# Performance work log

Hardware: AMD Instinct MI355X
Metric: run time of the kernel (lower is better)

## Reference

```python
import jax, jax.numpy as jnp
import numpy as np

N_HEAD = 32
N_KV_HEAD = 8
HEAD_DIM = 64
ROPE_THETA = 10000.0


def apply_rope(x):
    # x: [B, H, T, D], interleaved-pair RoPE (rotary_embedding_torch style)
    B, H, T, D = x.shape
    inv_freq = 1.0 / (ROPE_THETA ** (jnp.arange(0, D, 2, dtype=jnp.float32) / D))  # [D/2]
    ang = jnp.arange(T, dtype=jnp.float32)[:, None] * inv_freq[None, :]  # [T, D/2]
    cos = jnp.cos(ang)[None, None].astype(x.dtype)  # [1,1,T,D/2]
    sin = jnp.sin(ang)[None, None].astype(x.dtype)
    xe = x[..., 0::2]
    xo = x[..., 1::2]
    re = xe * cos - xo * sin
    ro = xo * cos + xe * sin
    return jnp.stack([re, ro], axis=-1).reshape(B, H, T, D)


def setup_inputs() -> dict:
    key = jax.random.key(0)
    ks = jax.random.split(key, 5)
    B, T, C = 2, 2048, 2048
    kv_dim = N_KV_HEAD * HEAD_DIM
    s = 0.02
    return {
        "x": jax.random.normal(ks[0], (B, T, C), jnp.float32),
        "wq": jax.random.normal(ks[1], (C, C), jnp.float32) * s,
        "wk": jax.random.normal(ks[2], (C, kv_dim), jnp.float32) * s,
        "wv": jax.random.normal(ks[3], (C, kv_dim), jnp.float32) * s,
        "wo": jax.random.normal(ks[4], (C, C), jnp.float32) * s,
    }


def reference(x, wq, wk, wv, wo):
    B, T, C = x.shape
    hd = HEAD_DIM
    q = (x @ wq).reshape(B, T, N_HEAD, hd).transpose(0, 2, 1, 3)      # [B,H,T,d]
    k = (x @ wk).reshape(B, T, N_KV_HEAD, hd).transpose(0, 2, 1, 3)   # [B,Hkv,T,d]
    v = (x @ wv).reshape(B, T, N_KV_HEAD, hd).transpose(0, 2, 1, 3)
    q = apply_rope(q)
    k = apply_rope(k)
    rep = N_HEAD // N_KV_HEAD
    k = jnp.repeat(k, rep, axis=1)  # repeat_interleave over head dim
    v = jnp.repeat(v, rep, axis=1)
    att = jnp.einsum('bhqd,bhkd->bhqk', q, k) * (1.0 / np.sqrt(hd))
    causal = jnp.tril(jnp.ones((T, T), dtype=bool))
    att = jnp.where(causal[None, None], att, jnp.finfo(att.dtype).min)
    att = jax.nn.softmax(att, axis=-1)
    y = jnp.einsum('bhqk,bhkd->bhqd', att, v)
    y = y.transpose(0, 2, 1, 3).reshape(B, T, C)
    return y @ wo
```

## Files before the change

kernel.cpp:

```cpp
#include <hip/hip_runtime.h>
#include <hip/hip_bf16.h>
#include <cstdint>
#include <cstddef>


using bf16 = __hip_bfloat16;
using f32x4  = __attribute__((ext_vector_type(4))) float;
using f32x16 = __attribute__((ext_vector_type(16))) float;
using short8 = __attribute__((ext_vector_type(8))) short;
using u32x4  = __attribute__((ext_vector_type(4))) unsigned int;

typedef __attribute__((address_space(1))) const void* gp1_t;
typedef __attribute__((address_space(3))) void*       lp3_t;

#define GLOAD_LDS16(g, l)                                                     \
  __builtin_amdgcn_global_load_lds((gp1_t)(const void*)(g), (lp3_t)(void*)(l), 16, 0, 0)

#define MFMA32(a, b, c) __builtin_amdgcn_mfma_f32_32x32x16_bf16(a, b, c, 0, 0, 0)

static constexpr int Bd  = 2;
static constexpr int Td  = 2048;
static constexpr int Cd  = 2048;
static constexpr int NH  = 32;
static constexpr int NKV = 8;
static constexpr int HD  = 64;
static constexpr int Md  = Bd * Td;

__device__ inline float bf2f(unsigned short u) {
  union { unsigned int i; float f; } v; v.i = ((unsigned int)u) << 16; return v.f;
}
__device__ inline unsigned short f2bfbits(float f) {
  union { float f; unsigned int u; } v; v.f = f;
  unsigned int r = v.u + 0x7fffu + ((v.u >> 16) & 1u);
  return (unsigned short)(r >> 16);
}
__device__ inline unsigned int pkbf(float a, float b) {
  unsigned int r;
  asm("v_cvt_pk_bf16_f32 %0, %1, %2" : "=v"(r) : "v"(a), "v"(b));
  return r;
}
__device__ inline void plswapf(float& a, float& b) {
  asm("v_permlane32_swap_b32 %0, %1" : "+v"(a), "+v"(b));
}
__device__ inline void plswapu(unsigned int& a, unsigned int& b) {
  asm("v_permlane32_swap_b32 %0, %1" : "+v"(a), "+v"(b));
}
__device__ inline float hmax16(const f32x16& v) {
  float a0 = fmaxf(v[0], v[1]),   a1 = fmaxf(v[2], v[3]);
  float a2 = fmaxf(v[4], v[5]),   a3 = fmaxf(v[6], v[7]);
  float a4 = fmaxf(v[8], v[9]),   a5 = fmaxf(v[10], v[11]);
  float a6 = fmaxf(v[12], v[13]), a7 = fmaxf(v[14], v[15]);
  float b0 = fmaxf(a0, a1), b1 = fmaxf(a2, a3);
  float b2 = fmaxf(a4, a5), b3 = fmaxf(a6, a7);
  return fmaxf(fmaxf(b0, b1), fmaxf(b2, b3));
}
__device__ inline float hsum16(const f32x16& v) {
  float a0 = v[0]+v[1],   a1 = v[2]+v[3],   a2 = v[4]+v[5],   a3 = v[6]+v[7];
  float a4 = v[8]+v[9],   a5 = v[10]+v[11], a6 = v[12]+v[13], a7 = v[14]+v[15];
  float b0 = a0+a1, b1 = a2+a3, b2 = a4+a5, b3 = a6+a7;
  return (b0+b1)+(b2+b3);
}

__global__ __launch_bounds__(256) void prep1_kernel(const float* __restrict__ x,
                                                    const float* __restrict__ wq,
                                                    const float* __restrict__ wk,
                                                    const float* __restrict__ wv,
                                                    bf16* __restrict__ xb,
                                                    bf16* __restrict__ w1) {
  __shared__ float tile[32][33];
  int bid = blockIdx.x, tid = threadIdx.x;
  if (bid < 8192) {
    int i = bid * 256 + tid;
    float4 v = ((const float4*)x)[i];
    ushort4 o;
    o.x = f2bfbits(v.x); o.y = f2bfbits(v.y); o.z = f2bfbits(v.z); o.w = f2bfbits(v.w);
    ((ushort4*)xb)[i] = o;
    return;
  }
  const float* in; bf16* out; int Cc, bx, by;
  if (bid < 12288)      { int l = bid - 8192;  in = wq; out = w1;                        Cc = 2048; bx = l & 63; by = l >> 6; }
  else if (bid < 13312) { int l = bid - 12288; in = wk; out = w1 + (size_t)2048 * 2048;  Cc = 512;  bx = l & 15; by = l >> 4; }
  else                  { int l = bid - 13312; in = wv; out = w1 + (size_t)2560 * 2048;  Cc = 512;  bx = l & 15; by = l >> 4; }
  int tx = tid & 31, ty = tid >> 5;
  int col = bx * 32 + tx;
#pragma unroll
  for (int i = 0; i < 4; ++i) {
    int row = by * 32 + ty + i * 8;
    tile[ty + i * 8][tx] = in[(size_t)row * Cc + col];
  }
  __syncthreads();
#pragma unroll
  for (int i = 0; i < 4; ++i) {
    int orow = bx * 32 + ty + i * 8;
    int ocol = by * 32 + tx;
    out[(size_t)orow * 2048 + ocol] = __float2bfloat16(tile[tx][ty + i * 8]);
  }
}

__global__ __launch_bounds__(256) void transpose_f2b(const float* __restrict__ in,
                                                     bf16* __restrict__ out,
                                                     int R, int Cc) {
  __shared__ float tile[32][33];
  int tx = threadIdx.x & 31, ty = threadIdx.x >> 5;
  int bx = blockIdx.x, by = blockIdx.y;
  int col = bx * 32 + tx;
#pragma unroll
  for (int i = 0; i < 4; ++i) {
    int row = by * 32 + ty + i * 8;
    tile[ty + i * 8][tx] = in[(size_t)row * Cc + col];
  }
  __syncthreads();
#pragma unroll
  for (int i = 0; i < 4; ++i) {
    int orow = bx * 32 + ty + i * 8;
    int ocol = by * 32 + tx;
    out[(size_t)orow * R + ocol] = __float2bfloat16(tile[tx][ty + i * 8]);
  }
}

template <int MODE>
__global__ __launch_bounds__(256, 2) void gemm_bf16(const bf16* __restrict__ A,
                                                    const bf16* __restrict__ Bt,
                                                    void* __restrict__ Cp,
                                                    int M, int N, int K) {
  __shared__ __align__(16) bf16 Al[2][128 * 64];
  __shared__ __align__(16) bf16 Bl[2][128 * 64];
  int tid = threadIdx.x;
  int w = tid >> 6, lane = tid & 63;
  int lr = lane & 15, lg = lane >> 4;
  int m0 = blockIdx.x * 128, n0 = blockIdx.y * 128;
  int wr = w >> 1, wc = w & 1;
  f32x4 acc[4][4] = {};

  size_t Kb = (size_t)K * 2;
  int c8 = lane & 7, r8 = lane >> 3;
  const char* Asrc = (const char*)A + (size_t)(m0 + w * 8 + r8) * Kb + ((c8 ^ r8) << 4);
  const char* Bsrc = (const char*)Bt + (size_t)(n0 + w * 8 + r8) * Kb + ((c8 ^ r8) << 4);

#define GSTAGE(kt, bb) do {                                                   \
    char* ald = (char*)&Al[bb][0] + w * 1024;                                 \
    char* bld = (char*)&Bl[bb][0] + w * 1024;                                 \
    _Pragma("unroll")                                                         \
    for (int j = 0; j < 4; ++j) {                                             \
      GLOAD_LDS16(Asrc + (size_t)j * 32 * Kb + (size_t)(kt) * 2, ald + j * 4096); \
      GLOAD_LDS16(Bsrc + (size_t)j * 32 * Kb + (size_t)(kt) * 2, bld + j * 4096); \
    }                                                                         \
  } while (0)

  int nkt = K >> 6;
  GSTAGE(0, 0);
  asm volatile("s_waitcnt vmcnt(0)" ::: "memory");
  __builtin_amdgcn_s_barrier();
  __builtin_amdgcn_sched_barrier(0);

  for (int t = 0; t < nkt; ++t) {
    int cur = t & 1;
    if (t + 1 < nkt) {
      GSTAGE((t + 1) << 6, cur ^ 1);
      asm volatile("s_waitcnt vmcnt(8)" ::: "memory");
    } else {
      asm volatile("s_waitcnt vmcnt(0)" ::: "memory");
    }
    __builtin_amdgcn_s_barrier();
    __builtin_amdgcn_sched_barrier(0);
    const char* Ab = (const char*)&Al[cur][0];
    const char* Bb = (const char*)&Bl[cur][0];
    __builtin_amdgcn_s_setprio(1);
#pragma unroll
    for (int kk = 0; kk < 2; ++kk) {
      short8 af[4], bfr[4];
#pragma unroll
      for (int f = 0; f < 4; ++f) {
        int ra = wr * 64 + f * 16 + lr;
        int rb = wc * 64 + f * 16 + lr;
        int cb = (((kk << 2) | lg) ^ (lr & 7)) << 4;
        af[f]  = *(const short8*)(Ab + (size_t)ra * 128 + cb);
        bfr[f] = *(const short8*)(Bb + (size_t)rb * 128 + cb);
      }
#pragma unroll
      for (int i = 0; i < 4; ++i)
#pragma unroll
        for (int j = 0; j < 4; ++j)
          acc[i][j] = __builtin_amdgcn_mfma_f32_16x16x32_bf16(af[i], bfr[j], acc[i][j], 0, 0, 0);
    }
    __builtin_amdgcn_s_setprio(0);
    asm volatile("s_waitcnt lgkmcnt(0)" ::: "memory");
    __builtin_amdgcn_sched_barrier(0);
    __builtin_amdgcn_s_barrier();
  }
#undef GSTAGE

  bf16* Qb  = (bf16*)Cp;
  bf16* Kb2 = Qb + (size_t)Bd * NH * Td * HD;
  bf16* Vtb = Kb2 + (size_t)Bd * NKV * Td * HD;

  if (MODE == 3 && n0 >= 2560) {
    int h  = (n0 - 2560 + wc * 64) >> 6;
    int b  = m0 >> 11;
    int tg = (m0 & 2047) + wr * 64;
    char* tb = (w < 2 ? (char*)&Al[0][0] : (char*)&Bl[0][0]) + (w & 1) * 8192;
#pragma unroll
    for (int i = 0; i < 4; ++i)
#pragma unroll
      for (int j = 0; j < 4; ++j)
#pragma unroll
        for (int r = 0; r < 4; r += 2) {
          int d  = j * 16 + lr;
          int tt = i * 16 + lg * 4 + r;
          unsigned int pk = pkbf(acc[i][j][r], acc[i][j][r + 1]);
          *(unsigned int*)(tb + (((size_t)d * 128 + tt * 2) ^ ((d & 7) << 4))) = pk;
        }
    asm volatile("s_waitcnt lgkmcnt(0)" ::: "memory");
    __builtin_amdgcn_sched_barrier(0);
    char* Vdst = (char*)Vtb + ((((size_t)b * NKV + h) * 64) * Td + tg) * 2;
#pragma unroll
    for (int p = 0; p < 8; ++p) {
      int d  = p * 8 + (lane >> 3);
      int tc = lane & 7;
      u32x4 v = *(const u32x4*)(tb + (((size_t)d * 128 + tc * 16) ^ ((d & 7) << 4)));
      *(u32x4*)(Vdst + (size_t)d * Td * 2 + tc * 16) = v;
    }
    return;
  }

  if (MODE == 3) {
    const float RC = -0.41524101186092029f;
    float sc = (n0 < 2048) ? 0.18033688011112042f : 1.0f;
    int odd = lane & 1;
#pragma unroll
    for (int j = 0; j < 4; ++j) {
      int ncol = n0 + wc * 64 + j * 16 + lr;
      int d  = ncol & 63;
      float inv = __builtin_amdgcn_exp2f((float)(d >> 1) * RC);
#pragma unroll
      for (int i = 0; i < 4; ++i) {
#pragma unroll
        for (int r = 0; r < 4; ++r) {
          int mrow = m0 + wr * 64 + i * 16 + lg * 4 + r;
          int t = mrow & 2047;
          float v = acc[i][j][r];
          float p = __shfl_xor(v, 1);
          float rev = (float)t * inv * 0.15915494309189535f;
          rev = rev - floorf(rev);
          float s = __builtin_amdgcn_sinf(rev);
          float c = __builtin_amdgcn_cosf(rev);
          float res = odd ? (v * c + p * s) : (v * c - p * s);
          res *= sc;
          int b = mrow >> 11;
          if (n0 < 2048) {
            int h = ncol >> 6;
            Qb[(((size_t)b * NH + h) * Td + t) * HD + d] = __float2bfloat16(res);
          } else {
            int h = (ncol - 2048) >> 6;
            Kb2[(((size_t)b * NKV + h) * Td + t) * HD + d] = __float2bfloat16(res);
          }
        }
      }
    }
    return;
  }

#pragma unroll
  for (int i = 0; i < 4; ++i)
#pragma unroll
    for (int j = 0; j < 4; ++j)
#pragma unroll
      for (int r = 0; r < 4; ++r) {
        int mrow = m0 + wr * 64 + i * 16 + lg * 4 + r;
        int ncol = n0 + wc * 64 + j * 16 + lr;
        ((float*)Cp)[(size_t)mrow * N + ncol] = acc[i][j][r];
      }
}

__global__ __launch_bounds__(512, 4) void attn_kernel(const bf16* __restrict__ Q,
                                                      const bf16* __restrict__ K,
                                                      const bf16* __restrict__ Vt,
                                                      bf16* __restrict__ Y) {
  __shared__ __align__(16) char lds[2 * 16384];
  int tid = threadIdx.x, w = tid >> 6, lane = tid & 63;
  int lq = lane & 31;
  int H  = lane >> 5;
  int qb = 7 - (int)blockIdx.y;
  int bh = blockIdx.x;
  int b = bh >> 5, h = bh & 31, kvh = h >> 2;
  int q0w = qb * 256 + w * 32;
  int qg  = q0w + lq;
  int tmax = qb * 4 + (w >> 1);
  int Nt   = qb * 4 + 4;

  const bf16* Qp = Q + (((size_t)b * NH + h) * Td) * HD;
  const char* Kg = (const char*)(K + (((size_t)b * NKV + kvh) * Td) * HD);
  const char* Vg = (const char*)(Vt + (((size_t)b * NKV + kvh) * HD) * Td);

  short8 qf[4];
#pragma unroll
  for (int ck = 0; ck < 4; ++ck)
    qf[ck] = *(const short8*)(Qp + (size_t)qg * HD + ck * 16 + H * 8);

  int srow   = lane >> 3;
  int scol16 = ((lane & 7) ^ srow) << 4;
  const char* Ksrc0 = Kg + (size_t)(w * 8 + srow) * 128 + scol16;
  const char* Vsrc0 = Vg + (size_t)(w * 8 + srow) * 4096 + scol16;
  char* KldsW[2] = { lds + w * 1024,          lds + 16384 + w * 1024 };
  char* VldsW[2] = { lds + 8192 + w * 1024,   lds + 24576 + w * 1024 };

#define STAGE_KV(tt, bb) do {                                                 \
    GLOAD_LDS16(Ksrc0 + (size_t)(tt) * 64 * 128, KldsW[bb]);                  \
    GLOAD_LDS16(Vsrc0 + (size_t)(tt) * 128,      VldsW[bb]);                  \
  } while (0)

  f32x16 acc0 = {}, acc1 = {};
  float m = -3e38f, l = 0.0f;
  int swz = (lq & 7) << 4;
  int rb0 = lq * 128, rb1 = (32 + lq) * 128;

  STAGE_KV(0, 0);
  asm volatile("s_waitcnt vmcnt(0)" ::: "memory");
  __syncthreads();

  for (int t = 0; t < Nt; ++t) {
    int cur = t & 1;
    if (t + 1 < Nt) STAGE_KV(t + 1, cur ^ 1);
    if (t <= tmax) {
      const char* Kl = lds + cur * 16384;
      const char* Vl = Kl + 8192;
      f32x16 s0 = {}, s1 = {};
      __builtin_amdgcn_s_setprio(1);
#pragma unroll
      for (int ck = 0; ck < 4; ++ck) {
        int c = (H * 16 + ck * 32) ^ swz;
        short8 kf0 = *(const short8*)(Kl + rb0 + c);
        short8 kf1 = *(const short8*)(Kl + rb1 + c);
        s0 = MFMA32(kf0, qf[ck], s0);
        s1 = MFMA32(kf1, qf[ck], s1);
      }
      __builtin_amdgcn_s_setprio(0);
      if (t == tmax) {
        int kvb = t * 64;
#pragma unroll
        for (int rr = 0; rr < 16; ++rr) {
          int krel = (rr & 3) + 8 * (rr >> 2) + 4 * H;
          if (kvb + krel > qg)      s0[rr] = -3e38f;
          if (kvb + 32 + krel > qg) s1[rr] = -3e38f;
        }
      }
      float mx = fmaxf(hmax16(s0), hmax16(s1));
      {
        float mb = mx;
        asm("" : "+v"(mb));
        plswapf(mx, mb);
        mx = fmaxf(mx, mb);
      }
      if (__any(mx > m + 8.0f)) {
        float mn = fmaxf(m, mx);
        float al = __builtin_amdgcn_exp2f(m - mn);
        m = mn;
        l *= al;
#pragma unroll
        for (int rr = 0; rr < 16; ++rr) { acc0[rr] *= al; acc1[rr] *= al; }
      }
#pragma unroll
      for (int rr = 0; rr < 16; ++rr) {
        s0[rr] = __builtin_amdgcn_exp2f(s0[rr] - m);
        s1[rr] = __builtin_amdgcn_exp2f(s1[rr] - m);
      }
      float ps = hsum16(s0) + hsum16(s1);
      {
        float pb = ps;
        asm("" : "+v"(pb));
        plswapf(ps, pb);
        ps += pb;
      }
      l += ps;
      short8 pf[4];
#pragma unroll
      for (int tt = 0; tt < 2; ++tt) {
        const f32x16& sv = tt ? s1 : s0;
#pragma unroll
        for (int a2 = 0; a2 < 2; ++a2) {
          unsigned int A0 = pkbf(sv[8*a2 + 0], sv[8*a2 + 1]);
          unsigned int A1 = pkbf(sv[8*a2 + 2], sv[8*a2 + 3]);
          unsigned int B0 = pkbf(sv[8*a2 + 4], sv[8*a2 + 5]);
          unsigned int B1 = pkbf(sv[8*a2 + 6], sv[8*a2 + 7]);
          plswapu(A0, B0);
          plswapu(A1, B1);
          u32x4 t4;
          t4[0] = A0; t4[1] = A1; t4[2] = B0; t4[3] = B1;
          pf[2*tt + a2] = __builtin_bit_cast(short8, t4);
        }
      }
      __builtin_amdgcn_s_setprio(1);
#pragma unroll
      for (int ks = 0; ks < 4; ++ks) {
        int c = (H * 16 + ks * 32) ^ swz;
        short8 vf0 = *(const short8*)(Vl + rb0 + c);
        short8 vf1 = *(const short8*)(Vl + rb1 + c);
        acc0 = MFMA32(vf0, pf[ks], acc0);
        acc1 = MFMA32(vf1, pf[ks], acc1);
      }
      __builtin_amdgcn_s_setprio(0);
    }
    asm volatile("s_waitcnt vmcnt(0)" ::: "memory");
    __syncthreads();
  }
#undef STAGE_KV

  float rn = 1.0f / l;
  bf16* Yp = Y + ((size_t)b * Td + qg) * Cd + h * HD;
#pragma unroll
  for (int rr = 0; rr < 16; rr += 2) {
    int d = (rr & 3) + 8 * (rr >> 2) + 4 * H;
    unsigned int w0 = pkbf(acc0[rr] * rn, acc0[rr + 1] * rn);
    unsigned int w1 = pkbf(acc1[rr] * rn, acc1[rr + 1] * rn);
    *(unsigned int*)(Yp + d)      = w0;
    *(unsigned int*)(Yp + 32 + d) = w1;
  }
}

extern "C" void kernel_launch(void* const* d_in, const int* in_sizes, int n_in,
                              void* d_out, int out_size, void* d_ws, size_t ws_size,
                              hipStream_t stream) {
  const float* x  = (const float*)d_in[0];
  const float* wq = (const float*)d_in[1];
  const float* wk = (const float*)d_in[2];
  const float* wv = (const float*)d_in[3];
  const float* wo = (const float*)d_in[4];

  char* ws = (char*)d_ws;
  const size_t o_xb = 0;
  const size_t o_w1 = o_xb + (size_t)Md * Cd * 2;
  const size_t o_Q  = o_w1 + (size_t)3072 * Cd * 2;
  const size_t o_K  = o_Q + (size_t)Bd * NH * Td * HD * 2;
  const size_t o_V  = o_K + (size_t)Bd * NKV * Td * HD * 2;

  bf16* xb  = (bf16*)(ws + o_xb);
  bf16* w1  = (bf16*)(ws + o_w1);
  bf16* Qb  = (bf16*)(ws + o_Q);
  bf16* Kb  = (bf16*)(ws + o_K);
  bf16* Vtb = (bf16*)(ws + o_V);
  bf16* yb  = xb;

  prep1_kernel<<<dim3(14336), dim3(256), 0, stream>>>(x, wq, wk, wv, xb, w1);
  gemm_bf16<3><<<dim3(Md / 128, 3072 / 128), dim3(256), 0, stream>>>(xb, w1, Qb, Md, 3072, Cd);
  transpose_f2b<<<dim3(Cd / 32, Cd / 32), dim3(256), 0, stream>>>(wo, w1, Cd, Cd);
  attn_kernel<<<dim3(Bd * NH, 8), dim3(512), 0, stream>>>(Qb, Kb, Vtb, yb);
  gemm_bf16<2><<<dim3(Md / 128, Cd / 128), dim3(256), 0, stream>>>(yb, w1, d_out, Md, Cd, Cd);
}
```

Baseline: 198.1 us.

## Enlarge GEMM tiles to 256x256 with 8 waves and phased MFMA scheduling

Retiles both bf16 GEMMs from 128x128 blocks of 256 threads to 256x256 blocks of 512 threads, using a 128KB double-buffered LDS region. Each wave now computes a 128x64 sub-tile in four barrier-separated MFMA phases, interleaving LDS fragment loads with the compute. The epilogues (RoPE Q/K scatter, V transpose via LDS, fp32 output store) are extended to the larger tile. The aim is more data reuse per LDS byte and fewer global loads per FLOP. The cost is far fewer blocks (192 and 128 on a 256-CU part), so many CUs sit idle and each CU holds only one block.

New measurement: 212.0 us. 1.07x slower.

```diff
diff --git a/kernel.cpp b/kernel.cpp
--- a/kernel.cpp
+++ b/kernel.cpp
@@ -16,6 +16,7 @@
 #define GLOAD_LDS16(g, l)                                                     \
   __builtin_amdgcn_global_load_lds((gp1_t)(const void*)(g), (lp3_t)(void*)(l), 16, 0, 0)
 
+#define MFMA16(a, b, c) __builtin_amdgcn_mfma_f32_16x16x32_bf16(a, b, c, 0, 0, 0)
 #define MFMA32(a, b, c) __builtin_amdgcn_mfma_f32_32x32x16_bf16(a, b, c, 0, 0, 0)
 
 static constexpr int Bd  = 2;
@@ -119,31 +120,32 @@
 }
 
 template <int MODE>
-__global__ __launch_bounds__(256, 2) void gemm_bf16(const bf16* __restrict__ A,
+__global__ __launch_bounds__(512, 2) void gemm_bf16(const bf16* __restrict__ A,
                                                     const bf16* __restrict__ Bt,
                                                     void* __restrict__ Cp,
                                                     int M, int N, int K) {
-  __shared__ __align__(16) bf16 Al[2][128 * 64];
-  __shared__ __align__(16) bf16 Bl[2][128 * 64];
+  __shared__ __align__(16) char lds[131072];
   int tid = threadIdx.x;
   int w = tid >> 6, lane = tid & 63;
   int lr = lane & 15, lg = lane >> 4;
-  int m0 = blockIdx.x * 128, n0 = blockIdx.y * 128;
-  int wr = w >> 1, wc = w & 1;
-  f32x4 acc[4][4] = {};
+  int m0 = blockIdx.x * 256, n0 = blockIdx.y * 256;
+  int wr = w >> 2, wc = w & 3;
+  f32x4 acc[8][4] = {};
 
   size_t Kb = (size_t)K * 2;
   int c8 = lane & 7, r8 = lane >> 3;
   const char* Asrc = (const char*)A + (size_t)(m0 + w * 8 + r8) * Kb + ((c8 ^ r8) << 4);
   const char* Bsrc = (const char*)Bt + (size_t)(n0 + w * 8 + r8) * Kb + ((c8 ^ r8) << 4);
+  char* AldsW = lds + w * 1024;
+  char* BldsW = lds + 65536 + w * 1024;
 
 #define GSTAGE(kt, bb) do {                                                   \
-    char* ald = (char*)&Al[bb][0] + w * 1024;                                 \
-    char* bld = (char*)&Bl[bb][0] + w * 1024;                                 \
     _Pragma("unroll")                                                         \
     for (int j = 0; j < 4; ++j) {                                             \
-      GLOAD_LDS16(Asrc + (size_t)j * 32 * Kb + (size_t)(kt) * 2, ald + j * 4096); \
-      GLOAD_LDS16(Bsrc + (size_t)j * 32 * Kb + (size_t)(kt) * 2, bld + j * 4096); \
+      GLOAD_LDS16(Asrc + (size_t)j * 64 * Kb + (size_t)(kt) * 2,              \
+                  AldsW + (bb) * 32768 + j * 8192);                           \
+      GLOAD_LDS16(Bsrc + (size_t)j * 64 * Kb + (size_t)(kt) * 2,              \
+                  BldsW + (bb) * 32768 + j * 8192);                           \
     }                                                                         \
   } while (0)
 
@@ -151,41 +153,83 @@
   GSTAGE(0, 0);
   asm volatile("s_waitcnt vmcnt(0)" ::: "memory");
   __builtin_amdgcn_s_barrier();
-  __builtin_amdgcn_sched_barrier(0);
 
   for (int t = 0; t < nkt; ++t) {
     int cur = t & 1;
-    if (t + 1 < nkt) {
-      GSTAGE((t + 1) << 6, cur ^ 1);
-      asm volatile("s_waitcnt vmcnt(8)" ::: "memory");
-    } else {
-      asm volatile("s_waitcnt vmcnt(0)" ::: "memory");
+    const char* Ab = lds + cur * 32768;
+    const char* Bb = lds + 65536 + cur * 32768;
+    short8 af[4][2], bfr[4][2];
+
+    if (t + 1 < nkt) GSTAGE((t + 1) << 6, cur ^ 1);
+#pragma unroll
+    for (int kk = 0; kk < 2; ++kk) {
+      int cb = (((kk << 2) | lg) ^ (lr & 7)) << 4;
+#pragma unroll
+      for (int f = 0; f < 4; ++f) {
+        af[f][kk]  = *(const short8*)(Ab + (size_t)(wr * 128 + f * 16 + lr) * 128 + cb);
+        bfr[f][kk] = *(const short8*)(Bb + (size_t)(wc * 64 + f * 16 + lr) * 128 + cb);
+      }
     }
     __builtin_amdgcn_s_barrier();
-    __builtin_amdgcn_sched_barrier(0);
-    const char* Ab = (const char*)&Al[cur][0];
-    const char* Bb = (const char*)&Bl[cur][0];
+    asm volatile("s_waitcnt lgkmcnt(0)" ::: "memory");
+    __builtin_amdgcn_sched_barrier(0);
     __builtin_amdgcn_s_setprio(1);
 #pragma unroll
+    for (int f = 0; f < 4; ++f)
+#pragma unroll
+      for (int g = 0; g < 2; ++g)
+#pragma unroll
+        for (int kk = 0; kk < 2; ++kk)
+          acc[f][g] = MFMA16(af[f][kk], bfr[g][kk], acc[f][g]);
+    __builtin_amdgcn_s_setprio(0);
+    __builtin_amdgcn_sched_barrier(0);
+    __builtin_amdgcn_s_barrier();
+
+    __builtin_amdgcn_s_setprio(1);
+#pragma unroll
+    for (int f = 0; f < 4; ++f)
+#pragma unroll
+      for (int g = 2; g < 4; ++g)
+#pragma unroll
+        for (int kk = 0; kk < 2; ++kk)
+          acc[f][g] = MFMA16(af[f][kk], bfr[g][kk], acc[f][g]);
+    __builtin_amdgcn_s_setprio(0);
+    __builtin_amdgcn_sched_barrier(0);
+    __builtin_amdgcn_s_barrier();
+
+#pragma unroll
     for (int kk = 0; kk < 2; ++kk) {
-      short8 af[4], bfr[4];
-#pragma unroll
-      for (int f = 0; f < 4; ++f) {
-        int ra = wr * 64 + f * 16 + lr;
-        int rb = wc * 64 + f * 16 + lr;
-        int cb = (((kk << 2) | lg) ^ (lr & 7)) << 4;
-        af[f]  = *(const short8*)(Ab + (size_t)ra * 128 + cb);
-        bfr[f] = *(const short8*)(Bb + (size_t)rb * 128 + cb);
-      }
-#pragma unroll
-      for (int i = 0; i < 4; ++i)
-#pragma unroll
-        for (int j = 0; j < 4; ++j)
-          acc[i][j] = __builtin_amdgcn_mfma_f32_16x16x32_bf16(af[i], bfr[j], acc[i][j], 0, 0, 0);
+      int cb = (((kk << 2) | lg) ^ (lr & 7)) << 4;
+#pragma unroll
+      for (int f = 0; f < 4; ++f)
+        af[f][kk] = *(const short8*)(Ab + (size_t)(wr * 128 + 64 + f * 16 + lr) * 128 + cb);
     }
+    __builtin_amdgcn_s_barrier();
+    asm volatile("s_waitcnt lgkmcnt(0)" ::: "memory");
+    __builtin_amdgcn_sched_barrier(0);
+    __builtin_amdgcn_s_setprio(1);
+#pragma unroll
+    for (int f = 0; f < 4; ++f)
+#pragma unroll
+      for (int g = 0; g < 2; ++g)
+#pragma unroll
+        for (int kk = 0; kk < 2; ++kk)
+          acc[4 + f][g] = MFMA16(af[f][kk], bfr[g][kk], acc[4 + f][g]);
     __builtin_amdgcn_s_setprio(0);
-    asm volatile("s_waitcnt lgkmcnt(0)" ::: "memory");
-    __builtin_amdgcn_sched_barrier(0);
+    __builtin_amdgcn_sched_barrier(0);
+    __builtin_amdgcn_s_barrier();
+
+    __builtin_amdgcn_s_setprio(1);
+#pragma unroll
+    for (int f = 0; f < 4; ++f)
+#pragma unroll
+      for (int g = 2; g < 4; ++g)
+#pragma unroll
+        for (int kk = 0; kk < 2; ++kk)
+          acc[4 + f][g] = MFMA16(af[f][kk], bfr[g][kk], acc[4 + f][g]);
+    __builtin_amdgcn_s_setprio(0);
+    __builtin_amdgcn_sched_barrier(0);
+    asm volatile("s_waitcnt vmcnt(0)" ::: "memory");
     __builtin_amdgcn_s_barrier();
   }
 #undef GSTAGE
@@ -195,12 +239,12 @@
   bf16* Vtb = Kb2 + (size_t)Bd * NKV * Td * HD;
 
   if (MODE == 3 && n0 >= 2560) {
+    int b  = m0 >> 11;
+    int tg = (m0 & 2047) + wr * 128;
     int h  = (n0 - 2560 + wc * 64) >> 6;
-    int b  = m0 >> 11;
-    int tg = (m0 & 2047) + wr * 64;
-    char* tb = (w < 2 ? (char*)&Al[0][0] : (char*)&Bl[0][0]) + (w & 1) * 8192;
-#pragma unroll
-    for (int i = 0; i < 4; ++i)
+    char* tb = lds + w * 16384;
+#pragma unroll
+    for (int i = 0; i < 8; ++i)
 #pragma unroll
       for (int j = 0; j < 4; ++j)
 #pragma unroll
@@ -208,16 +252,16 @@
           int d  = j * 16 + lr;
           int tt = i * 16 + lg * 4 + r;
           unsigned int pk = pkbf(acc[i][j][r], acc[i][j][r + 1]);
-          *(unsigned int*)(tb + (((size_t)d * 128 + tt * 2) ^ ((d & 7) << 4))) = pk;
+          *(unsigned int*)(tb + (((size_t)d * 256 + tt * 2) ^ ((d & 7) << 4))) = pk;
         }
     asm volatile("s_waitcnt lgkmcnt(0)" ::: "memory");
     __builtin_amdgcn_sched_barrier(0);
-    char* Vdst = (char*)Vtb + ((((size_t)b * NKV + h) * 64) * Td + tg) * 2;
-#pragma unroll
-    for (int p = 0; p < 8; ++p) {
-      int d  = p * 8 + (lane >> 3);
-      int tc = lane & 7;
-      u32x4 v = *(const u32x4*)(tb + (((size_t)d * 128 + tc * 16) ^ ((d & 7) << 4)));
+    char* Vdst = (char*)Vtb + (((size_t)(b * NKV + h) * 64) * Td + tg) * 2;
+#pragma unroll
+    for (int p = 0; p < 16; ++p) {
+      int d  = p * 4 + (lane >> 4);
+      int tc = lane & 15;
+      u32x4 v = *(const u32x4*)(tb + (((size_t)d * 256 + tc * 16) ^ ((d & 7) << 4)));
       *(u32x4*)(Vdst + (size_t)d * Td * 2 + tc * 16) = v;
     }
     return;
@@ -233,10 +277,10 @@
       int d  = ncol & 63;
       float inv = __builtin_amdgcn_exp2f((float)(d >> 1) * RC);
 #pragma unroll
-      for (int i = 0; i < 4; ++i) {
+      for (int i = 0; i < 8; ++i) {
 #pragma unroll
         for (int r = 0; r < 4; ++r) {
-          int mrow = m0 + wr * 64 + i * 16 + lg * 4 + r;
+          int mrow = m0 + wr * 128 + i * 16 + lg * 4 + r;
           int t = mrow & 2047;
           float v = acc[i][j][r];
           float p = __shfl_xor(v, 1);
@@ -261,12 +305,12 @@
   }
 
 #pragma unroll
-  for (int i = 0; i < 4; ++i)
+  for (int i = 0; i < 8; ++i)
 #pragma unroll
     for (int j = 0; j < 4; ++j)
 #pragma unroll
       for (int r = 0; r < 4; ++r) {
-        int mrow = m0 + wr * 64 + i * 16 + lg * 4 + r;
+        int mrow = m0 + wr * 128 + i * 16 + lg * 4 + r;
         int ncol = n0 + wc * 64 + j * 16 + lr;
         ((float*)Cp)[(size_t)mrow * N + ncol] = acc[i][j][r];
       }
@@ -441,8 +485,8 @@
   bf16* yb  = xb;
 
   prep1_kernel<<<dim3(14336), dim3(256), 0, stream>>>(x, wq, wk, wv, xb, w1);
-  gemm_bf16<3><<<dim3(Md / 128, 3072 / 128), dim3(256), 0, stream>>>(xb, w1, Qb, Md, 3072, Cd);
+  gemm_bf16<3><<<dim3(Md / 256, 3072 / 256), dim3(512), 0, stream>>>(xb, w1, Qb, Md, 3072, Cd);
   transpose_f2b<<<dim3(Cd / 32, Cd / 32), dim3(256), 0, stream>>>(wo, w1, Cd, Cd);
   attn_kernel<<<dim3(Bd * NH, 8), dim3(512), 0, stream>>>(Qb, Kb, Vtb, yb);
-  gemm_bf16<2><<<dim3(Md / 128, Cd / 128), dim3(256), 0, stream>>>(yb, w1, d_out, Md, Cd, Cd);
-}
+  gemm_bf16<2><<<dim3(Md / 256, Cd / 256), dim3(512), 0, stream>>>(yb, w1, d_out, Md, Cd, Cd);
+}
```
